# Performance work log

Measured on AMD Instinct MI355X. Metric: run time of the kernel, lower is better.

## Reference

```python
import jax, jax.numpy as jnp
import numpy as np

NUM_GRAPHS = 64

def setup_inputs() -> dict:
    key = jax.random.key(0)
    ks = jax.random.split(key, 8)
    N, E, F, H, C = 100000, 3200000, 512, 128, 2
    x = jax.random.normal(ks[0], (N, F), dtype=jnp.float32)
    edge_index = jax.random.randint(ks[1], (2, E), 0, N, dtype=jnp.int64)
    batch = jnp.sort(jax.random.randint(ks[2], (N,), 0, NUM_GRAPHS, dtype=jnp.int64))
    s = lambda k, sh, fan: jax.random.normal(k, sh, dtype=jnp.float32) / np.sqrt(fan)
    return {
        'x': x, 'edge_index': edge_index, 'batch': batch,
        'W1': s(ks[3], (F, H), F), 'b1': jnp.zeros((H,), jnp.float32),
        'W2': s(ks[4], (H, H), H), 'b2': jnp.zeros((H,), jnp.float32),
        'Wc': s(ks[5], (H, C), H), 'bc': jnp.zeros((C,), jnp.float32),
    }

def gcn_conv(x, W, b, src, dst, n_nodes):
    # PyG GCNConv: x' = D^-1/2 (A + I) D^-1/2 (x W) + b, deg counts self-loop
    h = x @ W                                            # [N, H]
    deg = jax.ops.segment_sum(jnp.ones_like(dst, dtype=h.dtype), dst,
                              num_segments=n_nodes) + 1.0  # +1 self-loop
    dinv = jax.lax.rsqrt(deg)                            # [N]
    coef = dinv[src] * dinv[dst]                         # [E]
    msg = h[src] * coef[:, None]                         # gather + scale
    agg = jax.ops.segment_sum(msg, dst, num_segments=n_nodes)
    agg = agg + h * (dinv * dinv)[:, None]               # self-loop term
    return agg + b

def reference(x, edge_index, batch, W1, b1, W2, b2, Wc, bc):
    N = x.shape[0]
    src, dst = edge_index[0], edge_index[1]
    h = jax.nn.relu(gcn_conv(x, W1, b1, src, dst, N))
    # dropout(0.5) is identity in eval mode
    h = jax.nn.relu(gcn_conv(h, W2, b2, src, dst, N))
    # global max pool per graph (batch is sorted)
    g = jax.ops.segment_max(h, batch, num_segments=NUM_GRAPHS,
                            indices_are_sorted=True)     # [G, H]
    return jax.nn.log_softmax(g @ Wc + bc, axis=-1)      # [G, C]
```

## Files before the change

### kernel.cpp

```cpp
#include <hip/hip_runtime.h>

typedef unsigned short u16;
typedef unsigned int   u32;
typedef __attribute__((ext_vector_type(4))) float f32x4;
typedef __attribute__((ext_vector_type(8))) short bf16x8;

#define NG 64
#define BSH 7
#define BCAP 5120
#define PAD 16

__device__ __forceinline__ u16 f2bf(float f){
  u32 u = __float_as_uint(f);
  u += 0x7fffu + ((u >> 16) & 1u);
  return (u16)(u >> 16);
}
__device__ __forceinline__ float bflo(u32 p){ return __uint_as_float(p << 16); }
__device__ __forceinline__ float bfhi(u32 p){ return __uint_as_float(p & 0xffff0000u); }

__global__ void bhist_kernel(const int* __restrict__ ei, int* __restrict__ bhist,
                             int E, int NBK){
  __shared__ int h[1024];
  int t = threadIdx.x;
  for (int b = t; b < 1024; b += 256) h[b] = 0;
  __syncthreads();
  for (int e = blockIdx.x * 256 + t; e < E; e += gridDim.x * 256)
    atomicAdd(&h[ei[E + e] >> BSH], 1);
  __syncthreads();
  for (int b = t; b < NBK; b += 256){
    int v = h[b];
    if (v) atomicAdd(&bhist[b * PAD], v);
  }
}

__global__ void bscan_kernel(const int* __restrict__ bhist, int* __restrict__ bbase,
                             int* __restrict__ gcur, int* __restrict__ rowptr,
                             int NBK, int E, int N){
  __shared__ int sh[256];
  int t = threadIdx.x;
  int base = t * 4;
  int v[4]; int s = 0;
  #pragma unroll
  for (int j = 0; j < 4; ++j){
    int idx = base + j;
    v[j] = (idx < NBK) ? bhist[idx * PAD] : 0;
    s += v[j];
  }
  sh[t] = s; __syncthreads();
  for (int off = 1; off < 256; off <<= 1){
    int x = sh[t]; int y = (t >= off) ? sh[t - off] : 0;
    __syncthreads(); sh[t] = x + y; __syncthreads();
  }
  int run = sh[t] - s;
  #pragma unroll
  for (int j = 0; j < 4; ++j){
    int idx = base + j;
    if (idx <= NBK){ bbase[idx * PAD] = run; gcur[idx * PAD] = run; }
    run += v[j];
  }
  if (t == 0) rowptr[N] = E;
}

__global__ void bin_kernel(const int* __restrict__ ei, int* __restrict__ gcur,
                           int2* __restrict__ mid, int E, int NBK){
  __shared__ int hist[1024];
  __shared__ int base[1024];
  int t = threadIdx.x;
  int e0 = blockIdx.x * 8192;
  int mysrc[32], mydst[32];
  for (int b = t; b < 1024; b += 256) hist[b] = 0;
  __syncthreads();
  #pragma unroll
  for (int i = 0; i < 32; ++i){
    int e = e0 + i * 256 + t;
    int d = -1, sv = 0;
    if (e < E){ d = ei[E + e]; sv = ei[e]; atomicAdd(&hist[d >> BSH], 1); }
    mydst[i] = d; mysrc[i] = sv;
  }
  __syncthreads();
  for (int b = t; b < NBK; b += 256){
    int hh = hist[b];
    if (hh) base[b] = atomicAdd(&gcur[b * PAD], hh);
  }
  __syncthreads();
  #pragma unroll
  for (int i = 0; i < 32; ++i){
    int d = mydst[i];
    if (d >= 0){
      int p = atomicAdd(&base[d >> BSH], 1);
      mid[p] = make_int2(mysrc[i], d);
    }
  }
}

__global__ void nodestat_kernel(const int2* __restrict__ mid, const int* __restrict__ bbase,
                                int* __restrict__ rowptr, float* __restrict__ dinv, int N){
  __shared__ int hist[128];
  __shared__ int sh[128];
  int b = blockIdx.x, t = threadIdx.x;
  int e0 = bbase[b * PAD], e1 = bbase[(b + 1) * PAD];
  if (t < 128) hist[t] = 0;
  __syncthreads();
  for (int i = e0 + t; i < e1; i += 256) atomicAdd(&hist[mid[i].y & 127], 1);
  __syncthreads();
  int val = (t < 128) ? hist[t] : 0;
  if (t < 128) sh[t] = val;
  __syncthreads();
  for (int off = 1; off < 128; off <<= 1){
    int x = 0;
    if (t < 128){ x = sh[t]; if (t >= off) x += sh[t - off]; }
    __syncthreads();
    if (t < 128) sh[t] = x;
    __syncthreads();
  }
  if (t < 128){
    int n = b * 128 + t;
    if (n < N){
      rowptr[n] = e0 + sh[t] - val;
      dinv[n] = rsqrtf((float)val + 1.0f);
    }
  }
}

__global__ __launch_bounds__(256)
void scatter_kernel(const int2* __restrict__ mid, const int* __restrict__ bbase,
                    const int* __restrict__ rowptr, const float* __restrict__ dinv,
                    int2* __restrict__ fin, int N){
  __shared__ int cur[128];
  __shared__ int2 stg[BCAP];
  int b = blockIdx.x, t = threadIdx.x;
  int e0 = bbase[b * PAD], e1 = bbase[(b + 1) * PAD];
  int sz = e1 - e0;
  if (t < 128){
    int n = b * 128 + t;
    cur[t] = ((n < N) ? rowptr[n] : e1) - e0;
  }
  __syncthreads();
  if (sz <= BCAP){
    for (int i = e0 + t; i < e1; i += 256){
      int2 m = mid[i];
      float w = dinv[m.x];
      int p = atomicAdd(&cur[m.y & 127], 1);
      stg[p] = make_int2(m.x, __float_as_int(w));
    }
    __syncthreads();
    for (int j = t; j < sz; j += 256) fin[e0 + j] = stg[j];
  } else {
    for (int i = e0 + t; i < e1; i += 256){
      int2 m = mid[i];
      float w = dinv[m.x];
      int p = atomicAdd(&cur[m.y & 127], 1);
      fin[e0 + p] = make_int2(m.x, __float_as_int(w));
    }
  }
}

__global__ void wcvt_kernel(const float* __restrict__ W1, const float* __restrict__ W2,
                            u16* __restrict__ W1T, u16* __restrict__ W2T){
  int i = blockIdx.x * 256 + threadIdx.x;
  if (i < 512 * 128){ int k = i >> 7, n = i & 127; W1T[(size_t)n * 512 + k] = f2bf(W1[i]); }
  if (i < 128 * 128){ int k = i >> 7, n = i & 127; W2T[(size_t)n * 128 + k] = f2bf(W2[i]); }
}

template<int A_BF16>
__global__ __launch_bounds__(256, 3)
void gemm_kernel(const void* __restrict__ Ap, const u16* __restrict__ BT,
                 u16* __restrict__ C, int N, int K)
{
  constexpr int LDA = 40;
  __shared__ __align__(16) u16 As[128 * LDA];
  __shared__ __align__(16) u16 Bs[128 * LDA];
  const int t = threadIdx.x;
  const int wave = t >> 6, lane = t & 63;
  const int q = lane >> 4, r = lane & 15;
  const int row0 = blockIdx.x * 128;
  f32x4 zero = {0.f, 0.f, 0.f, 0.f};
  f32x4 acc[2][8];
  #pragma unroll
  for (int i = 0; i < 2; ++i)
    #pragma unroll
    for (int j = 0; j < 8; ++j) acc[i][j] = zero;

  for (int k0 = 0; k0 < K; k0 += 32){
    {
      int rr = t >> 2, cc = (t & 3) * 8;
      #pragma unroll
      for (int it = 0; it < 2; ++it){
        int n = rr + it * 64;
        uint4 v = *(const uint4*)(BT + (size_t)n * K + k0 + cc);
        *(uint4*)(&Bs[n * LDA + cc]) = v;
      }
    }
    if (A_BF16){
      const u16* A = (const u16*)Ap;
      int rr = t >> 2, cc = (t & 3) * 8;
      #pragma unroll
      for (int it = 0; it < 2; ++it){
        int rl = rr + it * 64, row = row0 + rl;
        uint4 v = make_uint4(0u, 0u, 0u, 0u);
        if (row < N) v = *(const uint4*)(A + (size_t)row * K + k0 + cc);
        *(uint4*)(&As[rl * LDA + cc]) = v;
      }
    } else {
      const float* A = (const float*)Ap;
      int rr = t >> 3, cc = (t & 7) * 4;
      #pragma unroll
      for (int it = 0; it < 4; ++it){
        int rl = rr + it * 32, row = row0 + rl;
        float4 v = make_float4(0.f, 0.f, 0.f, 0.f);
        if (row < N) v = *(const float4*)(A + (size_t)row * K + k0 + cc);
        uint2 p;
        p.x = (u32)f2bf(v.x) | ((u32)f2bf(v.y) << 16);
        p.y = (u32)f2bf(v.z) | ((u32)f2bf(v.w) << 16);
        *(uint2*)(&As[rl * LDA + cc]) = p;
      }
    }
    __syncthreads();
    bf16x8 af[2], bfr[8];
    #pragma unroll
    for (int rt = 0; rt < 2; ++rt)
      af[rt] = *(const bf16x8*)(&As[(wave * 32 + rt * 16 + r) * LDA + q * 8]);
    #pragma unroll
    for (int ct = 0; ct < 8; ++ct)
      bfr[ct] = *(const bf16x8*)(&Bs[(ct * 16 + r) * LDA + q * 8]);
    #pragma unroll
    for (int rt = 0; rt < 2; ++rt)
      #pragma unroll
      for (int ct = 0; ct < 8; ++ct)
        acc[rt][ct] = __builtin_amdgcn_mfma_f32_16x16x32_bf16(af[rt], bfr[ct], acc[rt][ct], 0, 0, 0);
    __syncthreads();
  }
  #pragma unroll
  for (int rt = 0; rt < 2; ++rt)
    #pragma unroll
    for (int reg = 0; reg < 4; ++reg){
      int row = row0 + wave * 32 + rt * 16 + q * 4 + reg;
      if (row < N)
        #pragma unroll
        for (int ct = 0; ct < 8; ++ct)
          C[(size_t)row * 128 + ct * 16 + r] = f2bf(acc[rt][ct][reg]);
    }
}

__global__ __launch_bounds__(256)
void agg_kernel(const u16* __restrict__ h, const int2* __restrict__ edges,
                const int* __restrict__ rowptr, const float* __restrict__ dinv,
                const float* __restrict__ bias, u16* __restrict__ out, int N)
{
  int node = __builtin_amdgcn_readfirstlane((int)((blockIdx.x * 256 + threadIdx.x) >> 6));
  if (node >= N) return;
  const int lane = threadIdx.x & 63;
  const u32* __restrict__ hp = (const u32*)h;
  int beg = rowptr[node], end = rowptr[node + 1];

  u32 hs = hp[(size_t)node * 64 + lane];
  float dv = dinv[node];
  float b0 = bias[lane * 2 + 0], b1v = bias[lane * 2 + 1];

  float ax = 0.f, ay = 0.f;
  int2 pf[8];
  #pragma unroll
  for (int i = 0; i < 8; ++i){
    int idx = beg + i;
    pf[i] = (idx < end) ? edges[idx] : make_int2(0, 0);
  }
  for (int base = beg; base < end; base += 8){
    int2 cur[8];
    #pragma unroll
    for (int i = 0; i < 8; ++i) cur[i] = pf[i];
    #pragma unroll
    for (int i = 0; i < 8; ++i){
      int idx = base + 8 + i;
      pf[i] = (idx < end) ? edges[idx] : make_int2(0, 0);
    }
    u32 v[8];
    #pragma unroll
    for (int i = 0; i < 8; ++i)
      v[i] = hp[(size_t)cur[i].x * 64 + lane];
    #pragma unroll
    for (int i = 0; i < 8; ++i){
      float w = __int_as_float(cur[i].y);
      ax = fmaf(w, bflo(v[i]), ax);
      ay = fmaf(w, bfhi(v[i]), ay);
    }
  }
  float dv2 = dv * dv;
  ax = fmaf(dv, ax, fmaf(dv2, bflo(hs), b0));
  ay = fmaf(dv, ay, fmaf(dv2, bfhi(hs), b1v));
  ax = fmaxf(ax, 0.f); ay = fmaxf(ay, 0.f);
  u32 pk = (u32)f2bf(ax) | ((u32)f2bf(ay) << 16);
  __builtin_nontemporal_store(pk, (u32*)(out + (size_t)node * 128 + lane * 2));
}

__global__ void pool_kernel(const u16* __restrict__ h, const int* __restrict__ batch,
                            float* __restrict__ g, int N)
{
  int graph = blockIdx.x >> 3, chunk = blockIdx.x & 7;
  int f = threadIdx.x;
  int lo = 0, hi = N;
  while (lo < hi){ int mid = (lo + hi) >> 1; if (batch[mid] < graph) lo = mid + 1; else hi = mid; }
  int s = lo;
  hi = N;
  while (lo < hi){ int mid = (lo + hi) >> 1; if (batch[mid] < graph + 1) lo = mid + 1; else hi = mid; }
  int epos = lo;
  int len = epos - s;
  if (len <= 0) return;
  int per = (len + 7) >> 3;
  int a = s + chunk * per;
  int b = a + per; if (b > epos) b = epos;
  float m = 0.f;
  for (int n = a; n < b; ++n)
    m = fmaxf(m, __uint_as_float(((u32)h[(size_t)n * 128 + f]) << 16));
  if (a < b) atomicMax((int*)&g[graph * 128 + f], __float_as_int(m));
}

__global__ void head_kernel(const float* __restrict__ g, const float* __restrict__ Wc,
                            const float* __restrict__ bc, float* __restrict__ out)
{
  int gg = threadIdx.x;
  if (gg >= NG) return;
  float l0 = bc[0], l1 = bc[1];
  for (int f = 0; f < 128; ++f){
    float v = g[gg * 128 + f];
    l0 = fmaf(v, Wc[f * 2 + 0], l0);
    l1 = fmaf(v, Wc[f * 2 + 1], l1);
  }
  float m = fmaxf(l0, l1);
  float lse = m + logf(__expf(l0 - m) + __expf(l1 - m));
  out[gg * 2 + 0] = l0 - lse;
  out[gg * 2 + 1] = l1 - lse;
}

extern "C" void kernel_launch(void* const* d_in, const int* in_sizes, int n_in,
                              void* d_out, int out_size, void* d_ws, size_t ws_size,
                              hipStream_t stream)
{
  const float* x   = (const float*)d_in[0];
  const int*   ei  = (const int*)  d_in[1];
  const int*  batch= (const int*)  d_in[2];
  const float* W1  = (const float*)d_in[3];
  const float* b1  = (const float*)d_in[4];
  const float* W2  = (const float*)d_in[5];
  const float* b2  = (const float*)d_in[6];
  const float* Wc  = (const float*)d_in[7];
  const float* bc  = (const float*)d_in[8];
  float* out = (float*)d_out;
  (void)n_in; (void)out_size; (void)ws_size;

  const int N = in_sizes[0] / 512;
  const int E = in_sizes[1] / 2;
  const int NBK = (N + 127) >> 7;

  char* w = (char*)d_ws;
  size_t o = 0;
  auto take = [&](size_t bytes)->char* {
    char* p = w + o; o = (o + bytes + 511) & ~(size_t)511; return p;
  };
  size_t hbytes = (size_t)N * 128 * 2;
  size_t mbytes = (size_t)E * 8;
  int*   bhist  = (int*)  take((size_t)(NBK + 2) * PAD * 4);
  int*   bbase  = (int*)  take((size_t)(NBK + 2) * PAD * 4);
  int*   gcur   = (int*)  take((size_t)(NBK + 2) * PAD * 4);
  int*   rowptr = (int*)  take((size_t)(N + 1) * 4);
  float* dinv   = (float*)take((size_t)N * 4);
  int2*  fin    = (int2*) take(mbytes);
  u16*   W1T    = (u16*)  take((size_t)512 * 128 * 2);
  u16*   W2T    = (u16*)  take((size_t)128 * 128 * 2);
  u16*   hA     = (u16*)  take(hbytes > mbytes ? hbytes : mbytes);
  u16*   hB     = (u16*)  take(hbytes);
  float* gpool  = (float*)take((size_t)NG * 128 * 4);
  int2*  mid    = (int2*)hA;

  hipMemsetAsync(bhist, 0, (size_t)(NBK + 2) * PAD * 4, stream);
  hipMemsetAsync(gpool, 0, (size_t)NG * 128 * 4, stream);

  bhist_kernel<<<256, 256, 0, stream>>>(ei, bhist, E, NBK);
  bscan_kernel<<<1, 256, 0, stream>>>(bhist, bbase, gcur, rowptr, NBK, E, N);
  bin_kernel<<<(E + 8191) / 8192, 256, 0, stream>>>(ei, gcur, mid, E, NBK);
  nodestat_kernel<<<NBK, 256, 0, stream>>>(mid, bbase, rowptr, dinv, N);
  scatter_kernel<<<NBK, 256, 0, stream>>>(mid, bbase, rowptr, dinv, fin, N);
  wcvt_kernel<<<256, 256, 0, stream>>>(W1, W2, W1T, W2T);

  const int GB = (N + 127) / 128;
  gemm_kernel<0><<<GB, 256, 0, stream>>>((const void*)x,  W1T, hA, N, 512);
  agg_kernel<<<(N * 64 + 255) / 256, 256, 0, stream>>>(hA, fin, rowptr, dinv, b1, hB, N);
  gemm_kernel<1><<<GB, 256, 0, stream>>>((const void*)hB, W2T, hA, N, 128);
  agg_kernel<<<(N * 64 + 255) / 256, 256, 0, stream>>>(hA, fin, rowptr, dinv, b2, hB, N);
  pool_kernel<<<NG * 8, 128, 0, stream>>>(hB, batch, gpool, N);
  head_kernel<<<1, 64, 0, stream>>>(gpool, Wc, bc, out);
}
```

Before: 740.2 us.

## Slice feature columns across blocks and drop edge weights from CSR

Aggregation now splits each node's 128 features into 8 column slices handled by separate blocks. Within a wave, 8 lane groups process different edges in parallel and are combined with xor shuffles. The CSR edge array stores only source indices, and the normalization weight is fetched from dinv during aggregation. This aims to raise edge-level parallelism and shrink edge storage, but it rereads indices once per slice and issues narrower 32-byte gathers.

```diff
diff --git a/kernel.cpp b/kernel.cpp
--- a/kernel.cpp
+++ b/kernel.cpp
@@ -124,10 +124,10 @@
 
 __global__ __launch_bounds__(256)
 void scatter_kernel(const int2* __restrict__ mid, const int* __restrict__ bbase,
-                    const int* __restrict__ rowptr, const float* __restrict__ dinv,
-                    int2* __restrict__ fin, int N){
+                    const int* __restrict__ rowptr,
+                    int* __restrict__ fin, int N){
   __shared__ int cur[128];
-  __shared__ int2 stg[BCAP];
+  __shared__ int stg[BCAP];
   int b = blockIdx.x, t = threadIdx.x;
   int e0 = bbase[b * PAD], e1 = bbase[(b + 1) * PAD];
   int sz = e1 - e0;
@@ -139,18 +139,16 @@
   if (sz <= BCAP){
     for (int i = e0 + t; i < e1; i += 256){
       int2 m = mid[i];
-      float w = dinv[m.x];
       int p = atomicAdd(&cur[m.y & 127], 1);
-      stg[p] = make_int2(m.x, __float_as_int(w));
+      stg[p] = m.x;
     }
     __syncthreads();
     for (int j = t; j < sz; j += 256) fin[e0 + j] = stg[j];
   } else {
     for (int i = e0 + t; i < e1; i += 256){
       int2 m = mid[i];
-      float w = dinv[m.x];
       int p = atomicAdd(&cur[m.y & 127], 1);
-      fin[e0 + p] = make_int2(m.x, __float_as_int(w));
+      fin[e0 + p] = m.x;
     }
   }
 }
@@ -243,53 +241,54 @@
 }
 
 __global__ __launch_bounds__(256)
-void agg_kernel(const u16* __restrict__ h, const int2* __restrict__ edges,
+void agg_kernel(const u16* __restrict__ h, const int* __restrict__ srcs,
                 const int* __restrict__ rowptr, const float* __restrict__ dinv,
-                const float* __restrict__ bias, u16* __restrict__ out, int N)
-{
-  int node = __builtin_amdgcn_readfirstlane((int)((blockIdx.x * 256 + threadIdx.x) >> 6));
+                const float* __restrict__ bias, u16* __restrict__ out,
+                int N, int nodeBlocks)
+{
+  int slice = blockIdx.x / nodeBlocks;
+  int nb    = blockIdx.x - slice * nodeBlocks;
+  int node  = nb * 4 + (int)(threadIdx.x >> 6);
   if (node >= N) return;
   const int lane = threadIdx.x & 63;
+  const int grp = lane >> 3;
+  const int sub = lane & 7;
+  const int sOff = slice * 8 + sub;
   const u32* __restrict__ hp = (const u32*)h;
   int beg = rowptr[node], end = rowptr[node + 1];
 
-  u32 hs = hp[(size_t)node * 64 + lane];
-  float dv = dinv[node];
-  float b0 = bias[lane * 2 + 0], b1v = bias[lane * 2 + 1];
-
   float ax = 0.f, ay = 0.f;
-  int2 pf[8];
-  #pragma unroll
-  for (int i = 0; i < 8; ++i){
-    int idx = beg + i;
-    pf[i] = (idx < end) ? edges[idx] : make_int2(0, 0);
-  }
-  for (int base = beg; base < end; base += 8){
-    int2 cur[8];
-    #pragma unroll
-    for (int i = 0; i < 8; ++i) cur[i] = pf[i];
-    #pragma unroll
-    for (int i = 0; i < 8; ++i){
-      int idx = base + 8 + i;
-      pf[i] = (idx < end) ? edges[idx] : make_int2(0, 0);
-    }
-    u32 v[8];
-    #pragma unroll
-    for (int i = 0; i < 8; ++i)
-      v[i] = hp[(size_t)cur[i].x * 64 + lane];
-    #pragma unroll
-    for (int i = 0; i < 8; ++i){
-      float w = __int_as_float(cur[i].y);
-      ax = fmaf(w, bflo(v[i]), ax);
-      ay = fmaf(w, bfhi(v[i]), ay);
-    }
-  }
-  float dv2 = dv * dv;
-  ax = fmaf(dv, ax, fmaf(dv2, bflo(hs), b0));
-  ay = fmaf(dv, ay, fmaf(dv2, bfhi(hs), b1v));
-  ax = fmaxf(ax, 0.f); ay = fmaxf(ay, 0.f);
-  u32 pk = (u32)f2bf(ax) | ((u32)f2bf(ay) << 16);
-  __builtin_nontemporal_store(pk, (u32*)(out + (size_t)node * 128 + lane * 2));
+  if (beg < end){
+    int e = beg + grp;
+    int srcCur = __builtin_nontemporal_load(&srcs[e < end ? e : end - 1]);
+    float wCur = (e < end) ? dinv[srcCur] : 0.f;
+    for (int base = beg; base < end; base += 8){
+      int en = base + 8 + grp;
+      int srcNxt = 0;
+      bool more = (base + 8 < end);
+      if (more) srcNxt = __builtin_nontemporal_load(&srcs[en < end ? en : end - 1]);
+      u32 v = hp[(size_t)srcCur * 64 + sOff];
+      float wNxt = (more && en < end) ? dinv[srcNxt] : 0.f;
+      ax = fmaf(wCur, bflo(v), ax);
+      ay = fmaf(wCur, bfhi(v), ay);
+      srcCur = srcNxt; wCur = wNxt;
+    }
+  }
+  #pragma unroll
+  for (int off = 8; off < 64; off <<= 1){
+    ax += __shfl_xor(ax, off, 64);
+    ay += __shfl_xor(ay, off, 64);
+  }
+  if (grp == 0){
+    float dv = dinv[node], dv2 = dv * dv;
+    u32 hs = hp[(size_t)node * 64 + sOff];
+    float b0 = bias[sOff * 2 + 0], b1v = bias[sOff * 2 + 1];
+    ax = fmaf(dv, ax, fmaf(dv2, bflo(hs), b0));
+    ay = fmaf(dv, ay, fmaf(dv2, bfhi(hs), b1v));
+    ax = fmaxf(ax, 0.f); ay = fmaxf(ay, 0.f);
+    u32 pk = (u32)f2bf(ax) | ((u32)f2bf(ay) << 16);
+    __builtin_nontemporal_store(pk, (u32*)out + (size_t)node * 64 + sOff);
+  }
 }
 
 __global__ void pool_kernel(const u16* __restrict__ h, const int* __restrict__ batch,
@@ -363,7 +362,7 @@
   int*   gcur   = (int*)  take((size_t)(NBK + 2) * PAD * 4);
   int*   rowptr = (int*)  take((size_t)(N + 1) * 4);
   float* dinv   = (float*)take((size_t)N * 4);
-  int2*  fin    = (int2*) take(mbytes);
+  int*   fin    = (int*)  take((size_t)E * 4);
   u16*   W1T    = (u16*)  take((size_t)512 * 128 * 2);
   u16*   W2T    = (u16*)  take((size_t)128 * 128 * 2);
   u16*   hA     = (u16*)  take(hbytes > mbytes ? hbytes : mbytes);
@@ -378,14 +377,15 @@
   bscan_kernel<<<1, 256, 0, stream>>>(bhist, bbase, gcur, rowptr, NBK, E, N);
   bin_kernel<<<(E + 8191) / 8192, 256, 0, stream>>>(ei, gcur, mid, E, NBK);
   nodestat_kernel<<<NBK, 256, 0, stream>>>(mid, bbase, rowptr, dinv, N);
-  scatter_kernel<<<NBK, 256, 0, stream>>>(mid, bbase, rowptr, dinv, fin, N);
+  scatter_kernel<<<NBK, 256, 0, stream>>>(mid, bbase, rowptr, fin, N);
   wcvt_kernel<<<256, 256, 0, stream>>>(W1, W2, W1T, W2T);
 
   const int GB = (N + 127) / 128;
+  const int nodeBlocks = (N + 3) / 4;
   gemm_kernel<0><<<GB, 256, 0, stream>>>((const void*)x,  W1T, hA, N, 512);
-  agg_kernel<<<(N * 64 + 255) / 256, 256, 0, stream>>>(hA, fin, rowptr, dinv, b1, hB, N);
+  agg_kernel<<<8 * nodeBlocks, 256, 0, stream>>>(hA, fin, rowptr, dinv, b1, hB, N, nodeBlocks);
   gemm_kernel<1><<<GB, 256, 0, stream>>>((const void*)hB, W2T, hA, N, 128);
-  agg_kernel<<<(N * 64 + 255) / 256, 256, 0, stream>>>(hA, fin, rowptr, dinv, b2, hB, N);
+  agg_kernel<<<8 * nodeBlocks, 256, 0, stream>>>(hA, fin, rowptr, dinv, b2, hB, N, nodeBlocks);
   pool_kernel<<<NG * 8, 128, 0, stream>>>(hB, batch, gpool, N);
   head_kernel<<<1, 64, 0, stream>>>(gpool, Wc, bc, out);
 }
```

Measured after the change: 1.714 ms. +131.6%, slower.
